# Kernel optimization log

Measured on AMD Instinct MI355X. Metric: run time of the kernel, lower is better.

Reference implementation:

```python
import jax, jax.numpy as jnp
import numpy as np

B, S, H = 2, 1024, 2048          # batch, seq, hidden_size
I = 7168                          # intermediate_size
E = 8                             # num_local_experts
TOPK = 2                          # num_experts_per_tok
R = int(I * H * 0.1 / (I + H))    # delta_low_rank = 159


def setup_inputs() -> dict:
    key = jax.random.key(0)
    ks = jax.random.split(key, 12)
    s = 0.02
    return {
        "hidden_states": jax.random.normal(ks[0], (B, S, H), jnp.float32),
        "gate_w": jax.random.normal(ks[1], (E, H), jnp.float32) * s,
        "W1": jax.random.normal(ks[2], (E, I, H), jnp.float32) * s,
        "W2": jax.random.normal(ks[3], (E, H, I), jnp.float32) * s,
        "W3": jax.random.normal(ks[4], (E, I, H), jnp.float32) * s,
        "U1": jax.random.normal(ks[5], (E, I, R), jnp.float32) * s,
        "V1": jax.random.normal(ks[6], (E, R, H), jnp.float32) * s,
        "U2": jax.random.normal(ks[7], (E, H, R), jnp.float32) * s,
        "V2": jax.random.normal(ks[8], (E, R, I), jnp.float32) * s,
        "U3": jax.random.normal(ks[9], (E, I, R), jnp.float32) * s,
        "V3": jax.random.normal(ks[10], (E, R, H), jnp.float32) * s,
    }


def reference(hidden_states, gate_w, W1, W2, W3, U1, V1, U2, V2, U3, V3):
    b, s, h = hidden_states.shape
    x = hidden_states.reshape(-1, h)                     # [T, H]
    T = x.shape[0]
    router_logits = x @ gate_w.T                          # [T, E]
    probs = jax.nn.softmax(router_logits.astype(jnp.float32), axis=-1)
    rw, sel = jax.lax.top_k(probs, TOPK)                  # [T, k]
    rw = rw / jnp.sum(rw, axis=-1, keepdims=True)
    rw = rw.astype(x.dtype)
    # dense combine weights: zero for unselected experts (same math as gather/scatter)
    comb = jnp.zeros((T, E), x.dtype).at[jnp.arange(T)[:, None], sel].add(rw)
    out = jnp.zeros_like(x)
    for e in range(E):                                    # small fixed expert loop
        up = x @ W3[e].T + (x @ V3[e].T) @ U3[e].T        # [T, I]
        gate = x @ W1[e].T + (x @ V1[e].T) @ U1[e].T      # [T, I]
        hmid = jax.nn.silu(gate) * up                     # [T, I]
        y = hmid @ W2[e].T + (hmid @ V2[e].T) @ U2[e].T   # [T, H]
        out = out + comb[:, e, None] * y
    return out.reshape(b, s, h), router_logits
```

## Files before the change

kernel.cpp:

```cpp
#include <hip/hip_runtime.h>
#include <cstdint>
#include <cstddef>

#define TT 2048
#define HH 2048
#define II 7168
#define EE 8
#define RR 159
#define RPAD 192
#define ROWS 4096

typedef __attribute__((ext_vector_type(8))) short bf16x8;
typedef __attribute__((ext_vector_type(4))) float f32x4;

__device__ __forceinline__ unsigned short f2bf(float f) {
  unsigned int u = __float_as_uint(f);
  u += 0x7fffu + ((u >> 16) & 1u);
  return (unsigned short)(u >> 16);
}
__device__ __forceinline__ float bf2f(unsigned short u) {
  return __uint_as_float(((unsigned int)u) << 16);
}
__device__ __forceinline__ unsigned int cvtpk(float lo, float hi) {
  unsigned int r;
  asm volatile("v_cvt_pk_bf16_f32 %0, %1, %2" : "=v"(r) : "v"(lo), "v"(hi));
  return r;
}
__device__ __forceinline__ bf16x8 zero8() {
  bf16x8 v;
#pragma unroll
  for (int j = 0; j < 8; j++) v[j] = 0;
  return v;
}
__device__ __forceinline__ void gload16(const unsigned short* g, unsigned short* l) {
  __builtin_amdgcn_global_load_lds(
      (const __attribute__((address_space(1))) unsigned int*)g,
      (__attribute__((address_space(3))) unsigned int*)l, 16, 0, 0);
}

__global__ __launch_bounds__(256) void k_f2bf_flat(const float* __restrict__ s,
                                                   unsigned short* __restrict__ d,
                                                   long long n8) {
  long long i = (long long)blockIdx.x * blockDim.x + threadIdx.x;
  long long stride = (long long)gridDim.x * blockDim.x;
  for (; i < n8; i += stride) {
    const float* p = s + i * 8;
    float4 a = *(const float4*)p;
    float4 b = *(const float4*)(p + 4);
    bf16x8 v;
    v[0] = (short)f2bf(a.x); v[1] = (short)f2bf(a.y);
    v[2] = (short)f2bf(a.z); v[3] = (short)f2bf(a.w);
    v[4] = (short)f2bf(b.x); v[5] = (short)f2bf(b.y);
    v[6] = (short)f2bf(b.z); v[7] = (short)f2bf(b.w);
    *(bf16x8*)(d + i * 8) = v;
  }
}

__global__ __launch_bounds__(256) void k_upad(const float* __restrict__ U,
                                              unsigned short* __restrict__ Up, int rows) {
  long long idx = (long long)blockIdx.x * 256 + threadIdx.x;
  long long total = (long long)rows * 24;
  if (idx >= total) return;
  int row = (int)(idx / 24), c8 = (int)(idx % 24);
  unsigned short* dp = Up + (size_t)row * RPAD + c8 * 8;
#pragma unroll
  for (int j = 0; j < 8; j++) {
    int c = c8 * 8 + j;
    dp[j] = (c < RR) ? f2bf(U[(size_t)row * RR + c]) : (unsigned short)0;
  }
}

__global__ __launch_bounds__(256) void k_router(
    const float* __restrict__ x, const float* __restrict__ gw,
    float* __restrict__ logits_out, int* __restrict__ sel,
    float* __restrict__ wtok, int* __restrict__ counts) {
  int t = blockIdx.x;
  const float* xr = x + (size_t)t * HH;
  int base = threadIdx.x * 8;
  float4 x0 = *(const float4*)(xr + base);
  float4 x1 = *(const float4*)(xr + base + 4);
  float part[EE];
#pragma unroll
  for (int e = 0; e < EE; e++) {
    const float* g = gw + (size_t)e * HH + base;
    float4 g0 = *(const float4*)g;
    float4 g1 = *(const float4*)(g + 4);
    part[e] = x0.x * g0.x + x0.y * g0.y + x0.z * g0.z + x0.w * g0.w +
              x1.x * g1.x + x1.y * g1.y + x1.z * g1.z + x1.w * g1.w;
  }
#pragma unroll
  for (int off = 32; off > 0; off >>= 1)
#pragma unroll
    for (int e = 0; e < EE; e++) part[e] += __shfl_down(part[e], off);
  __shared__ float red[4][EE];
  int w = threadIdx.x >> 6, lane = threadIdx.x & 63;
  if (lane == 0) {
#pragma unroll
    for (int e = 0; e < EE; e++) red[w][e] = part[e];
  }
  __syncthreads();
  if (threadIdx.x == 0) {
    float lg[EE];
    float mx = -1e30f;
#pragma unroll
    for (int e = 0; e < EE; e++) {
      lg[e] = red[0][e] + red[1][e] + red[2][e] + red[3][e];
      logits_out[(size_t)t * EE + e] = lg[e];
      mx = fmaxf(mx, lg[e]);
    }
    float p[EE];
#pragma unroll
    for (int e = 0; e < EE; e++) p[e] = __expf(lg[e] - mx);
    int i0 = 0;
#pragma unroll
    for (int e = 1; e < EE; e++)
      if (lg[e] > lg[i0]) i0 = e;
    int i1 = (i0 == 0) ? 1 : 0;
#pragma unroll
    for (int e = 0; e < EE; e++)
      if (e != i0 && lg[e] > lg[i1]) i1 = e;
    float s = p[i0] + p[i1];
    sel[t * 2] = i0;
    sel[t * 2 + 1] = i1;
    wtok[t * 2] = p[i0] / s;
    wtok[t * 2 + 1] = p[i1] / s;
    atomicAdd(&counts[i0], 1);
    atomicAdd(&counts[i1], 1);
  }
}

__global__ void k_offsets(const int* __restrict__ counts, int* __restrict__ offs,
                          int* __restrict__ curs) {
  if (threadIdx.x == 0 && blockIdx.x == 0) {
    int o = 0;
    for (int e = 0; e < EE; e++) {
      offs[e] = o;
      curs[e] = o;
      o += counts[e];
    }
    offs[EE] = o;
  }
}

__global__ void k_build(const int* __restrict__ sel, const float* __restrict__ wtok,
                        int* __restrict__ curs, int* __restrict__ rowsA,
                        float* __restrict__ rowwgt, int* __restrict__ rowid) {
  int t = blockIdx.x * blockDim.x + threadIdx.x;
  if (t >= TT) return;
  for (int k = 0; k < 2; k++) {
    int e = sel[t * 2 + k];
    int pos = atomicAdd(&curs[e], 1);
    rowsA[pos] = t;
    rowwgt[pos] = wtok[t * 2 + k];
    rowid[t * 2 + k] = pos;
  }
}

__global__ void k_x2bf(const float* __restrict__ x, unsigned short* __restrict__ xb) {
  size_t i = (size_t)blockIdx.x * blockDim.x + threadIdx.x;
  size_t n8 = (size_t)TT * HH / 8;
  size_t stride = (size_t)gridDim.x * blockDim.x;
  for (size_t idx = i; idx < n8; idx += stride) {
    const float* s = x + idx * 8;
    float4 a = *(const float4*)s;
    float4 b = *(const float4*)(s + 4);
    bf16x8 v;
    v[0] = (short)f2bf(a.x); v[1] = (short)f2bf(a.y);
    v[2] = (short)f2bf(a.z); v[3] = (short)f2bf(a.w);
    v[4] = (short)f2bf(b.x); v[5] = (short)f2bf(b.y);
    v[6] = (short)f2bf(b.z); v[7] = (short)f2bf(b.w);
    *(bf16x8*)(xb + idx * 8) = v;
  }
}

template <bool GATHER>
__global__ __launch_bounds__(256, 2) void k_lowrank_sk(
    const unsigned short* __restrict__ Ab, int lda, int K, int kc, int NS,
    const unsigned short* __restrict__ V0, const unsigned short* __restrict__ V1,
    float* __restrict__ Pp,
    const int* __restrict__ counts, const int* __restrict__ offs,
    const int* __restrict__ rowsA) {
  int e = blockIdx.y;
  int cnt = counts[e];
  int m0 = blockIdx.x * 64;
  if (m0 >= cnt) return;
  int roff = offs[e];
  int mat = blockIdx.z / NS, split = blockIdx.z % NS;
  const unsigned short* V = ((mat == 0) ? V0 : V1) + (size_t)e * RR * K;
  float* Pout = Pp + (size_t)blockIdx.z * ROWS * RPAD;
  int kt0 = split * kc;
  int kt1 = kt0 + kc;
  if (kt1 > K) kt1 = K;
  __shared__ unsigned short As[64 * 64];
  __shared__ unsigned short Bs[192 * 64];
  int tid = threadIdx.x, lane = tid & 63, w = tid >> 6;
  int rstage = tid >> 3, cg = tid & 7;
  f32x4 acc[12];
#pragma unroll
  for (int n = 0; n < 12; n++) acc[n] = (f32x4){0.f, 0.f, 0.f, 0.f};
  for (int kt = kt0; kt < kt1; kt += 64) {
#pragma unroll
    for (int p = 0; p < 2; p++) {
      int r = p * 32 + rstage;
      bf16x8 v = zero8();
      int gr = m0 + r;
      if (gr < cnt) {
        size_t arow = GATHER ? (size_t)rowsA[roff + gr] : (size_t)(roff + gr);
        v = *(const bf16x8*)(Ab + arow * (size_t)lda + kt + cg * 8);
      }
      *(bf16x8*)&As[r * 64 + ((cg ^ (r & 7)) * 8)] = v;
    }
#pragma unroll
    for (int p = 0; p < 6; p++) {
      int r = p * 32 + rstage;
      bf16x8 v = zero8();
      if (r < RR) v = *(const bf16x8*)(V + (size_t)r * K + kt + cg * 8);
      *(bf16x8*)&Bs[r * 64 + ((cg ^ (r & 7)) * 8)] = v;
    }
    __syncthreads();
#pragma unroll
    for (int ks = 0; ks < 2; ks++) {
      int rA = w * 16 + (lane & 15);
      bf16x8 a = *(const bf16x8*)&As[rA * 64 + (((ks * 4 + (lane >> 4)) ^ (rA & 7)) * 8)];
#pragma unroll
      for (int n = 0; n < 12; n++) {
        int rB = n * 16 + (lane & 15);
        bf16x8 b = *(const bf16x8*)&Bs[rB * 64 + (((ks * 4 + (lane >> 4)) ^ (rB & 7)) * 8)];
        acc[n] = __builtin_amdgcn_mfma_f32_16x16x32_bf16(a, b, acc[n], 0, 0, 0);
      }
    }
    __syncthreads();
  }
  int mbase = m0 + w * 16 + (lane >> 4) * 4;
#pragma unroll
  for (int n = 0; n < 12; n++) {
    int col = n * 16 + (lane & 15);
#pragma unroll
    for (int r4 = 0; r4 < 4; r4++) {
      int row = mbase + r4;
      if (row < cnt) Pout[(size_t)(roff + row) * RPAD + col] = acc[n][r4];
    }
  }
}

__global__ __launch_bounds__(256) void k_lr_reduce(
    const float* __restrict__ Pp, unsigned short* __restrict__ P0,
    unsigned short* __restrict__ P1m, int NS, int nmat) {
  long long idx = (long long)blockIdx.x * 256 + threadIdx.x;
  long long total = (long long)nmat * ROWS * 24;
  if (idx >= total) return;
  int mat = (int)(idx / ((long long)ROWS * 24));
  int rem = (int)(idx % ((long long)ROWS * 24));
  int row = rem / 24, c8 = rem % 24;
  const float* base = Pp + ((size_t)mat * NS) * ROWS * RPAD + (size_t)row * RPAD + c8 * 8;
  float s0 = 0, s1 = 0, s2 = 0, s3 = 0, s4 = 0, s5 = 0, s6 = 0, s7 = 0;
  for (int sp = 0; sp < NS; sp++) {
    const float* p = base + (size_t)sp * ROWS * RPAD;
    float4 a = *(const float4*)p;
    float4 b = *(const float4*)(p + 4);
    s0 += a.x; s1 += a.y; s2 += a.z; s3 += a.w;
    s4 += b.x; s5 += b.y; s6 += b.z; s7 += b.w;
  }
  bf16x8 v;
  v[0] = (short)f2bf(s0); v[1] = (short)f2bf(s1);
  v[2] = (short)f2bf(s2); v[3] = (short)f2bf(s3);
  v[4] = (short)f2bf(s4); v[5] = (short)f2bf(s5);
  v[6] = (short)f2bf(s6); v[7] = (short)f2bf(s7);
  unsigned short* P = (mat == 0) ? P0 : P1m;
  *(bf16x8*)(P + (size_t)row * RPAD + c8 * 8) = v;
}

template <int MODE>
__global__ __launch_bounds__(256, 2) void k_gemm2(
    const unsigned short* __restrict__ Ab, int K, int N,
    const float* __restrict__ Wf,
    const unsigned short* __restrict__ Pq,
    const unsigned short* __restrict__ Uq,
    const unsigned short* __restrict__ Gb,
    const float* __restrict__ rowwgt,
    unsigned short* __restrict__ outb,
    float* __restrict__ outf,
    const int* __restrict__ counts, const int* __restrict__ offs,
    const int* __restrict__ rowsA) {
  int e = blockIdx.z;
  int cnt = counts[e];
  int m0 = blockIdx.y * 128;
  if (m0 >= cnt) return;
  int n0 = blockIdx.x * 128;
  int roff = offs[e];
  const float* w = Wf + (size_t)e * (size_t)N * K;
  const unsigned short* uq = Uq + (size_t)e * (size_t)N * RPAD;
  __shared__ unsigned short As[2][128 * 64];
  __shared__ unsigned short Bs[2][128 * 64];
  int tid = threadIdx.x, lane = tid & 63, wv = tid >> 6;
  int wr = (wv >> 1) * 64, wc = (wv & 1) * 64;
  f32x4 acc[4][4];
#pragma unroll
  for (int m = 0; m < 4; m++)
#pragma unroll
    for (int n = 0; n < 4; n++) acc[m][n] = (f32x4){0.f, 0.f, 0.f, 0.f};
  int srow = (wv << 5) + (lane >> 3);
  int swz = (((lane & 7) ^ ((lane >> 3) & 7)) << 3);
  int aoff[4], woff[4];
#pragma unroll
  for (int i = 0; i < 4; i++) {
    int gr = m0 + srow + i * 8;
    if (gr >= cnt) gr = cnt - 1;
    int arow = (MODE < 2) ? rowsA[roff + gr] : (roff + gr);
    aoff[i] = arow * K + swz;
    woff[i] = (n0 + srow + i * 8) * K + swz;
  }
  float4 rb[4][2];
#pragma unroll
  for (int i = 0; i < 4; i++) {
    gload16(Ab + aoff[i], &As[0][((wv << 5) + (i << 3)) * 64]);
    rb[i][0] = *(const float4*)(w + woff[i]);
    rb[i][1] = *(const float4*)(w + woff[i] + 4);
  }
#pragma unroll
  for (int i = 0; i < 4; i++) {
    int idx = (srow + i * 8) * 64 + (lane & 7) * 8;
    uint4 q;
    q.x = cvtpk(rb[i][0].x, rb[i][0].y);
    q.y = cvtpk(rb[i][0].z, rb[i][0].w);
    q.z = cvtpk(rb[i][1].x, rb[i][1].y);
    q.w = cvtpk(rb[i][1].z, rb[i][1].w);
    *(uint4*)&Bs[0][idx] = q;
  }
  __syncthreads();
  int nt = K >> 6;
  for (int t = 0; t < nt; ++t) {
    int cur = t & 1, nxt = cur ^ 1;
    bool more = (t + 1 < nt);
    if (more) {
#pragma unroll
      for (int i = 0; i < 4; i++) {
        gload16(Ab + aoff[i] + (t + 1) * 64, &As[nxt][((wv << 5) + (i << 3)) * 64]);
        rb[i][0] = *(const float4*)(w + woff[i] + (t + 1) * 64);
        rb[i][1] = *(const float4*)(w + woff[i] + (t + 1) * 64 + 4);
      }
    }
#pragma unroll
    for (int ks = 0; ks < 2; ks++) {
      bf16x8 af[4], bsr[4];
#pragma unroll
      for (int m = 0; m < 4; m++) {
        int r = wr + m * 16 + (lane & 15);
        af[m] = *(const bf16x8*)&As[cur][r * 64 + (((ks * 4 + (lane >> 4)) ^ (r & 7)) * 8)];
      }
#pragma unroll
      for (int n = 0; n < 4; n++) {
        int r = wc + n * 16 + (lane & 15);
        bsr[n] = *(const bf16x8*)&Bs[cur][r * 64 + (((ks * 4 + (lane >> 4)) ^ (r & 7)) * 8)];
      }
#pragma unroll
      for (int m = 0; m < 4; m++)
#pragma unroll
        for (int n = 0; n < 4; n++)
          acc[m][n] = __builtin_amdgcn_mfma_f32_16x16x32_bf16(af[m], bsr[n], acc[m][n], 0, 0, 0);
    }
    if (more) {
#pragma unroll
      for (int i = 0; i < 4; i++) {
        int idx = (srow + i * 8) * 64 + (lane & 7) * 8;
        uint4 q;
        q.x = cvtpk(rb[i][0].x, rb[i][0].y);
        q.y = cvtpk(rb[i][0].z, rb[i][0].w);
        q.z = cvtpk(rb[i][1].x, rb[i][1].y);
        q.w = cvtpk(rb[i][1].z, rb[i][1].w);
        *(uint4*)&Bs[nxt][idx] = q;
      }
    }
    __syncthreads();
  }
  for (int kt = 0; kt < RPAD; kt += 64) {
#pragma unroll
    for (int i = 0; i < 4; i++) {
      int gr = m0 + srow + i * 8;
      if (gr >= cnt) gr = cnt - 1;
      gload16(Pq + (size_t)(roff + gr) * RPAD + swz + kt, &As[0][((wv << 5) + (i << 3)) * 64]);
      gload16(uq + (size_t)(n0 + srow + i * 8) * RPAD + swz + kt,
              &Bs[0][((wv << 5) + (i << 3)) * 64]);
    }
    __syncthreads();
#pragma unroll
    for (int ks = 0; ks < 2; ks++) {
      bf16x8 af[4], bsr[4];
#pragma unroll
      for (int m = 0; m < 4; m++) {
        int r = wr + m * 16 + (lane & 15);
        af[m] = *(const bf16x8*)&As[0][r * 64 + (((ks * 4 + (lane >> 4)) ^ (r & 7)) * 8)];
      }
#pragma unroll
      for (int n = 0; n < 4; n++) {
        int r = wc + n * 16 + (lane & 15);
        bsr[n] = *(const bf16x8*)&Bs[0][r * 64 + (((ks * 4 + (lane >> 4)) ^ (r & 7)) * 8)];
      }
#pragma unroll
      for (int m = 0; m < 4; m++)
#pragma unroll
        for (int n = 0; n < 4; n++)
          acc[m][n] = __builtin_amdgcn_mfma_f32_16x16x32_bf16(af[m], bsr[n], acc[m][n], 0, 0, 0);
    }
    __syncthreads();
  }
#pragma unroll
  for (int m = 0; m < 4; m++) {
#pragma unroll
    for (int r4 = 0; r4 < 4; r4++) {
      int row = m0 + wr + m * 16 + (lane >> 4) * 4 + r4;
      if (row < cnt) {
        size_t rbase = (size_t)(roff + row) * N + n0 + wc;
        if constexpr (MODE == 0) {
#pragma unroll
          for (int n = 0; n < 4; n++)
            outb[rbase + n * 16 + (lane & 15)] = f2bf(acc[m][n][r4]);
        } else if constexpr (MODE == 1) {
#pragma unroll
          for (int n = 0; n < 4; n++) {
            float g = bf2f(Gb[rbase + n * 16 + (lane & 15)]);
            float uu = acc[m][n][r4];
            float h = (g / (1.f + __expf(-g))) * uu;
            outb[rbase + n * 16 + (lane & 15)] = f2bf(h);
          }
        } else {
          float wgt = rowwgt[roff + row];
#pragma unroll
          for (int n = 0; n < 4; n++)
            outf[rbase + n * 16 + (lane & 15)] = acc[m][n][r4] * wgt;
        }
      }
    }
  }
}

__global__ void k_combine(const float* __restrict__ ybuf, const int* __restrict__ rowid,
                          float* __restrict__ out) {
  int idx = blockIdx.x * 256 + threadIdx.x;
  int t = idx >> 8;
  int c = (idx & 255) * 8;
  int r0 = rowid[t * 2], r1 = rowid[t * 2 + 1];
  const float* y0 = ybuf + (size_t)r0 * HH + c;
  const float* y1 = ybuf + (size_t)r1 * HH + c;
  float4 a0 = *(const float4*)y0, a1 = *(const float4*)(y0 + 4);
  float4 b0 = *(const float4*)y1, b1 = *(const float4*)(y1 + 4);
  float4 o0 = {a0.x + b0.x, a0.y + b0.y, a0.z + b0.z, a0.w + b0.w};
  float4 o1 = {a1.x + b1.x, a1.y + b1.y, a1.z + b1.z, a1.w + b1.w};
  float* o = out + (size_t)t * HH + c;
  *(float4*)o = o0;
  *(float4*)(o + 4) = o1;
}

extern "C" void kernel_launch(void* const* d_in, const int* in_sizes, int n_in,
                              void* d_out, int out_size, void* d_ws, size_t ws_size,
                              hipStream_t stream) {
  const float* x  = (const float*)d_in[0];
  const float* gw = (const float*)d_in[1];
  const float* W1 = (const float*)d_in[2];
  const float* W2 = (const float*)d_in[3];
  const float* W3 = (const float*)d_in[4];
  const float* U1 = (const float*)d_in[5];
  const float* V1 = (const float*)d_in[6];
  const float* U2 = (const float*)d_in[7];
  const float* V2 = (const float*)d_in[8];
  const float* U3 = (const float*)d_in[9];
  const float* V3 = (const float*)d_in[10];
  float* out = (float*)d_out;
  float* logits = out + (size_t)TT * HH;

  char* ws = (char*)d_ws;
  size_t off = 0;
  auto take = [&](size_t b) -> char* {
    char* p = ws + off;
    off += (b + 255) & ~(size_t)255;
    return p;
  };
  unsigned short* Xb   = (unsigned short*)take((size_t)TT * HH * 2);
  unsigned short* hmid = (unsigned short*)take((size_t)ROWS * II * 2);
  unsigned short* Gbuf = (unsigned short*)take((size_t)ROWS * II * 2);
  unsigned short* P1   = (unsigned short*)take((size_t)ROWS * RPAD * 2);
  unsigned short* P3   = (unsigned short*)take((size_t)ROWS * RPAD * 2);
  unsigned short* P2   = (unsigned short*)take((size_t)ROWS * RPAD * 2);
  float* ybuf          = (float*)take((size_t)ROWS * HH * 4);
  int* sel             = (int*)take((size_t)TT * 2 * 4);
  float* wtok          = (float*)take((size_t)TT * 2 * 4);
  int* rowsA           = (int*)take((size_t)ROWS * 4);
  float* rowwgt        = (float*)take((size_t)ROWS * 4);
  int* rowid           = (int*)take((size_t)TT * 2 * 4);
  int* meta            = (int*)take(1024);
  int* counts  = meta;
  int* offs    = meta + 16;
  int* curs    = meta + 32;
  unsigned short* V1b = (unsigned short*)take((size_t)EE * RR * HH * 2);
  unsigned short* V3b = (unsigned short*)take((size_t)EE * RR * HH * 2);
  unsigned short* V2b = (unsigned short*)take((size_t)EE * RR * II * 2);
  unsigned short* U1p = (unsigned short*)take((size_t)EE * II * RPAD * 2);
  unsigned short* U3p = (unsigned short*)take((size_t)EE * II * RPAD * 2);
  unsigned short* U2p = (unsigned short*)take((size_t)EE * HH * RPAD * 2);
  float* Pp           = (float*)take((size_t)8 * ROWS * RPAD * 4);

  hipMemsetAsync(counts, 0, EE * sizeof(int), stream);
  k_f2bf_flat<<<1024, 256, 0, stream>>>(V1, V1b, (long long)EE * RR * HH / 8);
  k_f2bf_flat<<<1024, 256, 0, stream>>>(V3, V3b, (long long)EE * RR * HH / 8);
  k_f2bf_flat<<<1024, 256, 0, stream>>>(V2, V2b, (long long)EE * RR * II / 8);
  k_upad<<<(EE * II * 24 + 255) / 256, 256, 0, stream>>>(U1, U1p, EE * II);
  k_upad<<<(EE * II * 24 + 255) / 256, 256, 0, stream>>>(U3, U3p, EE * II);
  k_upad<<<(EE * HH * 24 + 255) / 256, 256, 0, stream>>>(U2, U2p, EE * HH);
  k_router<<<TT, 256, 0, stream>>>(x, gw, logits, sel, wtok, counts);
  k_offsets<<<1, 64, 0, stream>>>(counts, offs, curs);
  k_build<<<TT / 256, 256, 0, stream>>>(sel, wtok, curs, rowsA, rowwgt, rowid);
  k_x2bf<<<2048, 256, 0, stream>>>(x, Xb);
  k_lowrank_sk<true><<<dim3(TT / 64, EE, 2 * 4), 256, 0, stream>>>(
      Xb, HH, HH, 512, 4, V1b, V3b, Pp, counts, offs, rowsA);
  k_lr_reduce<<<(2 * ROWS * 24 + 255) / 256, 256, 0, stream>>>(Pp, P1, P3, 4, 2);
  k_gemm2<0><<<dim3(II / 128, TT / 128, EE), 256, 0, stream>>>(
      Xb, HH, II, W1, P1, U1p, nullptr, nullptr, Gbuf, nullptr, counts, offs, rowsA);
  k_gemm2<1><<<dim3(II / 128, TT / 128, EE), 256, 0, stream>>>(
      Xb, HH, II, W3, P3, U3p, Gbuf, nullptr, hmid, nullptr, counts, offs, rowsA);
  k_lowrank_sk<false><<<dim3(TT / 64, EE, 8), 256, 0, stream>>>(
      hmid, II, II, 896, 8, V2b, V2b, Pp, counts, offs, rowsA);
  k_lr_reduce<<<(ROWS * 24 + 255) / 256, 256, 0, stream>>>(Pp, P2, P2, 8, 1);
  k_gemm2<2><<<dim3(HH / 128, TT / 128, EE), 256, 0, stream>>>(
      hmid, II, HH, W2, P2, U2p, nullptr, rowwgt, nullptr, ybuf, counts, offs, rowsA);
  k_combine<<<(TT * HH / 8) / 256, 256, 0, stream>>>(ybuf, rowid, out);
}
```

Baseline: 1.378 ms.

## Fuse bf16 conversion of x into router and single-buffer weight tile in GEMM

The router kernel now also writes the bf16 copy of the activations, which removes the separate conversion kernel and one extra pass over x. The grouped GEMM uses a single LDS buffer for the converted fp32 weight tile: it converts and stores at the start of each K iteration, then syncs, instead of converting the next tile after the MFMAs into a double buffer. This reduces LDS usage, but the weight conversion is no longer overlapped with the compute of the previous tile, which may expose latency. The GEMM kernel is also renamed.

Result: faster. 1.197 ms (-13.1%).

```diff
diff --git a/kernel.cpp b/kernel.cpp
--- a/kernel.cpp
+++ b/kernel.cpp
@@ -73,12 +73,21 @@
 __global__ __launch_bounds__(256) void k_router(
     const float* __restrict__ x, const float* __restrict__ gw,
     float* __restrict__ logits_out, int* __restrict__ sel,
-    float* __restrict__ wtok, int* __restrict__ counts) {
+    float* __restrict__ wtok, int* __restrict__ counts,
+    unsigned short* __restrict__ xb) {
   int t = blockIdx.x;
   const float* xr = x + (size_t)t * HH;
   int base = threadIdx.x * 8;
   float4 x0 = *(const float4*)(xr + base);
   float4 x1 = *(const float4*)(xr + base + 4);
+  {
+    bf16x8 v;
+    v[0] = (short)f2bf(x0.x); v[1] = (short)f2bf(x0.y);
+    v[2] = (short)f2bf(x0.z); v[3] = (short)f2bf(x0.w);
+    v[4] = (short)f2bf(x1.x); v[5] = (short)f2bf(x1.y);
+    v[6] = (short)f2bf(x1.z); v[7] = (short)f2bf(x1.w);
+    *(bf16x8*)(xb + (size_t)t * HH + base) = v;
+  }
   float part[EE];
 #pragma unroll
   for (int e = 0; e < EE; e++) {
@@ -153,23 +162,6 @@
     rowsA[pos] = t;
     rowwgt[pos] = wtok[t * 2 + k];
     rowid[t * 2 + k] = pos;
-  }
-}
-
-__global__ void k_x2bf(const float* __restrict__ x, unsigned short* __restrict__ xb) {
-  size_t i = (size_t)blockIdx.x * blockDim.x + threadIdx.x;
-  size_t n8 = (size_t)TT * HH / 8;
-  size_t stride = (size_t)gridDim.x * blockDim.x;
-  for (size_t idx = i; idx < n8; idx += stride) {
-    const float* s = x + idx * 8;
-    float4 a = *(const float4*)s;
-    float4 b = *(const float4*)(s + 4);
-    bf16x8 v;
-    v[0] = (short)f2bf(a.x); v[1] = (short)f2bf(a.y);
-    v[2] = (short)f2bf(a.z); v[3] = (short)f2bf(a.w);
-    v[4] = (short)f2bf(b.x); v[5] = (short)f2bf(b.y);
-    v[6] = (short)f2bf(b.z); v[7] = (short)f2bf(b.w);
-    *(bf16x8*)(xb + idx * 8) = v;
   }
 }
 
@@ -271,7 +263,7 @@
 }
 
 template <int MODE>
-__global__ __launch_bounds__(256, 2) void k_gemm2(
+__global__ __launch_bounds__(256, 2) void k_gemm(
     const unsigned short* __restrict__ Ab, int K, int N,
     const float* __restrict__ Wf,
     const unsigned short* __restrict__ Pq,
@@ -291,7 +283,7 @@
   const float* w = Wf + (size_t)e * (size_t)N * K;
   const unsigned short* uq = Uq + (size_t)e * (size_t)N * RPAD;
   __shared__ unsigned short As[2][128 * 64];
-  __shared__ unsigned short Bs[2][128 * 64];
+  __shared__ unsigned short Bs[128 * 64];
   int tid = threadIdx.x, lane = tid & 63, wv = tid >> 6;
   int wr = (wv >> 1) * 64, wc = (wv & 1) * 64;
   f32x4 acc[4][4];
@@ -317,20 +309,20 @@
     rb[i][0] = *(const float4*)(w + woff[i]);
     rb[i][1] = *(const float4*)(w + woff[i] + 4);
   }
-#pragma unroll
-  for (int i = 0; i < 4; i++) {
-    int idx = (srow + i * 8) * 64 + (lane & 7) * 8;
-    uint4 q;
-    q.x = cvtpk(rb[i][0].x, rb[i][0].y);
-    q.y = cvtpk(rb[i][0].z, rb[i][0].w);
-    q.z = cvtpk(rb[i][1].x, rb[i][1].y);
-    q.w = cvtpk(rb[i][1].z, rb[i][1].w);
-    *(uint4*)&Bs[0][idx] = q;
-  }
-  __syncthreads();
   int nt = K >> 6;
   for (int t = 0; t < nt; ++t) {
     int cur = t & 1, nxt = cur ^ 1;
+#pragma unroll
+    for (int i = 0; i < 4; i++) {
+      int idx = (srow + i * 8) * 64 + (lane & 7) * 8;
+      uint4 q;
+      q.x = cvtpk(rb[i][0].x, rb[i][0].y);
+      q.y = cvtpk(rb[i][0].z, rb[i][0].w);
+      q.z = cvtpk(rb[i][1].x, rb[i][1].y);
+      q.w = cvtpk(rb[i][1].z, rb[i][1].w);
+      *(uint4*)&Bs[idx] = q;
+    }
+    __syncthreads();
     bool more = (t + 1 < nt);
     if (more) {
 #pragma unroll
@@ -351,25 +343,13 @@
 #pragma unroll
       for (int n = 0; n < 4; n++) {
         int r = wc + n * 16 + (lane & 15);
-        bsr[n] = *(const bf16x8*)&Bs[cur][r * 64 + (((ks * 4 + (lane >> 4)) ^ (r & 7)) * 8)];
+        bsr[n] = *(const bf16x8*)&Bs[r * 64 + (((ks * 4 + (lane >> 4)) ^ (r & 7)) * 8)];
       }
 #pragma unroll
       for (int m = 0; m < 4; m++)
 #pragma unroll
         for (int n = 0; n < 4; n++)
           acc[m][n] = __builtin_amdgcn_mfma_f32_16x16x32_bf16(af[m], bsr[n], acc[m][n], 0, 0, 0);
-    }
-    if (more) {
-#pragma unroll
-      for (int i = 0; i < 4; i++) {
-        int idx = (srow + i * 8) * 64 + (lane & 7) * 8;
-        uint4 q;
-        q.x = cvtpk(rb[i][0].x, rb[i][0].y);
-        q.y = cvtpk(rb[i][0].z, rb[i][0].w);
-        q.z = cvtpk(rb[i][1].x, rb[i][1].y);
-        q.w = cvtpk(rb[i][1].z, rb[i][1].w);
-        *(uint4*)&Bs[nxt][idx] = q;
-      }
     }
     __syncthreads();
   }
@@ -380,7 +360,7 @@
       if (gr >= cnt) gr = cnt - 1;
       gload16(Pq + (size_t)(roff + gr) * RPAD + swz + kt, &As[0][((wv << 5) + (i << 3)) * 64]);
       gload16(uq + (size_t)(n0 + srow + i * 8) * RPAD + swz + kt,
-              &Bs[0][((wv << 5) + (i << 3)) * 64]);
+              &Bs[((wv << 5) + (i << 3)) * 64]);
     }
     __syncthreads();
 #pragma unroll
@@ -394,7 +374,7 @@
 #pragma unroll
       for (int n = 0; n < 4; n++) {
         int r = wc + n * 16 + (lane & 15);
-        bsr[n] = *(const bf16x8*)&Bs[0][r * 64 + (((ks * 4 + (lane >> 4)) ^ (r & 7)) * 8)];
+        bsr[n] = *(const bf16x8*)&Bs[r * 64 + (((ks * 4 + (lane >> 4)) ^ (r & 7)) * 8)];
       }
 #pragma unroll
       for (int m = 0; m < 4; m++)
@@ -506,21 +486,20 @@
   k_upad<<<(EE * II * 24 + 255) / 256, 256, 0, stream>>>(U1, U1p, EE * II);
   k_upad<<<(EE * II * 24 + 255) / 256, 256, 0, stream>>>(U3, U3p, EE * II);
   k_upad<<<(EE * HH * 24 + 255) / 256, 256, 0, stream>>>(U2, U2p, EE * HH);
-  k_router<<<TT, 256, 0, stream>>>(x, gw, logits, sel, wtok, counts);
+  k_router<<<TT, 256, 0, stream>>>(x, gw, logits, sel, wtok, counts, Xb);
   k_offsets<<<1, 64, 0, stream>>>(counts, offs, curs);
   k_build<<<TT / 256, 256, 0, stream>>>(sel, wtok, curs, rowsA, rowwgt, rowid);
-  k_x2bf<<<2048, 256, 0, stream>>>(x, Xb);
   k_lowrank_sk<true><<<dim3(TT / 64, EE, 2 * 4), 256, 0, stream>>>(
       Xb, HH, HH, 512, 4, V1b, V3b, Pp, counts, offs, rowsA);
   k_lr_reduce<<<(2 * ROWS * 24 + 255) / 256, 256, 0, stream>>>(Pp, P1, P3, 4, 2);
-  k_gemm2<0><<<dim3(II / 128, TT / 128, EE), 256, 0, stream>>>(
+  k_gemm<0><<<dim3(II / 128, TT / 128, EE), 256, 0, stream>>>(
       Xb, HH, II, W1, P1, U1p, nullptr, nullptr, Gbuf, nullptr, counts, offs, rowsA);
-  k_gemm2<1><<<dim3(II / 128, TT / 128, EE), 256, 0, stream>>>(
+  k_gemm<1><<<dim3(II / 128, TT / 128, EE), 256, 0, stream>>>(
       Xb, HH, II, W3, P3, U3p, Gbuf, nullptr, hmid, nullptr, counts, offs, rowsA);
   k_lowrank_sk<false><<<dim3(TT / 64, EE, 8), 256, 0, stream>>>(
       hmid, II, II, 896, 8, V2b, V2b, Pp, counts, offs, rowsA);
   k_lr_reduce<<<(ROWS * 24 + 255) / 256, 256, 0, stream>>>(Pp, P2, P2, 8, 1);
-  k_gemm2<2><<<dim3(HH / 128, TT / 128, EE), 256, 0, stream>>>(
+  k_gemm<2><<<dim3(HH / 128, TT / 128, EE), 256, 0, stream>>>(
       hmid, II, HH, W2, P2, U2p, nullptr, rowwgt, nullptr, ybuf, counts, offs, rowsA);
   k_combine<<<(TT * HH / 8) / 256, 256, 0, stream>>>(ybuf, rowid, out);
 }
```
